# Kernel optimization log

Measured on AMD Instinct MI355X. Metric: run time of the kernel, lower is better.

The kernel has to match this reference:

```python
import jax, jax.numpy as jnp
import numpy as np

NUM_HOP = 3
VOCAB = 32000
D = 512          # embed_dim
MEM = 60         # memory_size (> story_size -> T_A slice branch)
BS = 64
STORY = 50
SENT = 32        # max_sent_size
QLEN = 16


def positional_encoding(J, d):
    # pe[i-1, k-1] = 1 - i/J - (k/d) * (1 - 2*i/J), i in 1..J, k in 1..d
    i = jnp.arange(1, J + 1, dtype=jnp.float32)[:, None]
    k = jnp.arange(1, d + 1, dtype=jnp.float32)[None, :]
    return 1.0 - i / J - (k / d) * (1.0 - 2.0 * i / J)


def setup_inputs() -> dict:
    key = jax.random.key(0)
    kA, kT, kC, kQ = jax.random.split(key, 4)
    # stacked embedding tables A[0..num_hop], each (VOCAB, D), N(0, 0.1)
    A = jax.random.normal(kA, (NUM_HOP + 1, VOCAB, D), dtype=jnp.float32) * 0.1
    T_A = jax.random.normal(kT, (1, MEM, D), dtype=jnp.float32) * 0.1
    context = jax.random.randint(kC, (BS, STORY, SENT), 0, VOCAB)
    query = jax.random.randint(kQ, (BS, QLEN), 0, VOCAB)
    return {"context": context, "query": query, "A": A, "T_A": T_A}


def reference(context, query, A, T_A):
    # padding_idx=0: row 0 of every table is zero
    A = A.at[:, 0, :].set(0.0)
    pe = positional_encoding(SENT, D)              # (SENT, D)

    # query encoding: u = B(query).sum(axis=1), B = A[0]; dropout is identity at eval
    u = A[0][query].sum(axis=1)                    # (BS, D)

    for h in range(NUM_HOP):
        # memory embedding with positional encoding, summed over words
        m = (A[h][context] * pe).sum(axis=2)       # (BS, STORY, D)
        # temporal encoding: memory_size > story_size branch
        m = m + T_A[:, :STORY, :]
        # output embedding (no positional encoding applied in original)
        c = A[h + 1][context].sum(axis=2)          # (BS, STORY, D)
        p = jax.nn.softmax(jnp.einsum('bsd,bd->bs', m, u), axis=1)
        u = u + jnp.einsum('bs,bsd->bd', p, c)

    # W = A[-1].weight.T -> logits = u @ W
    logits = u @ A[NUM_HOP].T                      # (BS, VOCAB)
    return jax.nn.softmax(logits, axis=-1)
```

## Files before the change

kernel.cpp:

```cpp
#include <hip/hip_runtime.h>
#include <math.h>

#define NUM_HOP 3
#define VOCAB   32000
#define DIM     512
#define MEM     60
#define BS      64
#define STORY   50
#define SENT    32
#define QLEN    16

#define SZ      ((size_t)BS * STORY * DIM)
#define TBL     ((size_t)VOCAB * DIM)

typedef short v8s __attribute__((ext_vector_type(8)));
typedef float v4f __attribute__((ext_vector_type(4)));

static __device__ __forceinline__ ushort f2bf(float x) {
    union { float f; unsigned u; } v; v.f = x;
    unsigned r = (v.u + 0x7FFFu + ((v.u >> 16) & 1u)) >> 16;
    return (ushort)r;
}

__global__ __launch_bounds__(128) void k_gather(const float* __restrict__ A,
                                                const int*   __restrict__ ctx,
                                                const int*   __restrict__ query,
                                                float*       __restrict__ mw,
                                                float*       __restrict__ c,
                                                float*       __restrict__ u) {
    const unsigned blk = blockIdx.x;
    const int d = threadIdx.x * 4;
    if (blk >= 4u * BS * STORY) {
        const int b = blk - 4u * BS * STORY;
        const int* q = query + b * QLEN;
        float4 acc = make_float4(0.f, 0.f, 0.f, 0.f);
        for (int t = 0; t < QLEN; ++t) {
            const int idx = q[t];
            if (idx != 0) {
                const float4 a = *(const float4*)(A + (size_t)idx * DIM + d);
                acc.x += a.x; acc.y += a.y; acc.z += a.z; acc.w += a.w;
            }
        }
        *(float4*)(u + (size_t)b * DIM + d) = acc;
        return;
    }
    const unsigned pass = blk / (BS * STORY);
    const unsigned bs   = blk - pass * (BS * STORY);
    const float* table = A + (size_t)pass * TBL;
    const int*   cw    = ctx + bs * SENT;

    float4 m  = make_float4(0.f, 0.f, 0.f, 0.f);
    float4 cc = make_float4(0.f, 0.f, 0.f, 0.f);
    const float invD = 1.0f / (float)DIM;
    #pragma unroll 8
    for (int w = 0; w < SENT; ++w) {
        const int idx = cw[w];
        if (idx == 0) continue;
        const float4 a = *(const float4*)(table + (size_t)idx * DIM + d);
        const float aw = 1.0f - (float)(w + 1) * (1.0f / (float)SENT);
        const float bw = 1.0f - (float)(2 * (w + 1)) * (1.0f / (float)SENT);
        m.x = fmaf(a.x, aw - bw * (float)(d + 1) * invD, m.x);
        m.y = fmaf(a.y, aw - bw * (float)(d + 2) * invD, m.y);
        m.z = fmaf(a.z, aw - bw * (float)(d + 3) * invD, m.z);
        m.w = fmaf(a.w, aw - bw * (float)(d + 4) * invD, m.w);
        cc.x += a.x; cc.y += a.y; cc.z += a.z; cc.w += a.w;
    }
    if (pass < 3) *(float4*)(mw + (size_t)pass * SZ + (size_t)bs * DIM + d) = m;
    if (pass > 0) *(float4*)(c + (size_t)(pass - 1) * SZ + (size_t)bs * DIM + d) = cc;
}

__global__ __launch_bounds__(512) void k_hops(const float* __restrict__ mw,
                                              const float* __restrict__ c,
                                              const float* __restrict__ T_A,
                                              const float* __restrict__ u_g,
                                              ushort*      __restrict__ ubf) {
    const int b    = blockIdx.x;
    const int tid  = threadIdx.x;
    const int wave = tid >> 6;
    const int lane = tid & 63;
    __shared__ float su[DIM];
    __shared__ float sw[64];
    __shared__ float up[8][DIM];

    su[tid] = u_g[(size_t)b * DIM + tid];
    __syncthreads();

    for (int h = 0; h < NUM_HOP; ++h) {
        const float* mwh = mw + (size_t)h * SZ + (size_t)b * STORY * DIM;
        const float* ch  = c  + (size_t)h * SZ + (size_t)b * STORY * DIM;

        const float4 u0 = *(const float4*)(&su[lane * 8]);
        const float4 u1 = *(const float4*)(&su[lane * 8 + 4]);
        for (int s = wave; s < STORY; s += 8) {
            const float* mrow = mwh + (size_t)s * DIM + lane * 8;
            const float* trow = T_A + (size_t)s * DIM + lane * 8;
            const float4 m0 = *(const float4*)(mrow);
            const float4 m1 = *(const float4*)(mrow + 4);
            const float4 t0 = *(const float4*)(trow);
            const float4 t1 = *(const float4*)(trow + 4);
            float p = (m0.x + t0.x) * u0.x + (m0.y + t0.y) * u0.y +
                      (m0.z + t0.z) * u0.z + (m0.w + t0.w) * u0.w +
                      (m1.x + t1.x) * u1.x + (m1.y + t1.y) * u1.y +
                      (m1.z + t1.z) * u1.z + (m1.w + t1.w) * u1.w;
            for (int off = 32; off; off >>= 1) p += __shfl_down(p, off);
            if (lane == 0) sw[s] = p;
        }
        __syncthreads();

        if (tid < 64) {
            const float v = (tid < STORY) ? sw[tid] : -1e30f;
            float mx = v;
            for (int off = 32; off; off >>= 1) mx = fmaxf(mx, __shfl_down(mx, off));
            mx = __shfl(mx, 0);
            const float e = (tid < STORY) ? __expf(v - mx) : 0.f;
            float sm = e;
            for (int off = 32; off; off >>= 1) sm += __shfl_down(sm, off);
            sm = __shfl(sm, 0);
            if (tid < STORY) sw[tid] = e / sm;
        }
        __syncthreads();

        float4 a0 = make_float4(0.f, 0.f, 0.f, 0.f);
        float4 a1 = make_float4(0.f, 0.f, 0.f, 0.f);
        for (int s = wave; s < STORY; s += 8) {
            const float  w    = sw[s];
            const float* crow = ch + (size_t)s * DIM + lane * 8;
            const float4 c0 = *(const float4*)(crow);
            const float4 c1 = *(const float4*)(crow + 4);
            a0.x = fmaf(w, c0.x, a0.x); a0.y = fmaf(w, c0.y, a0.y);
            a0.z = fmaf(w, c0.z, a0.z); a0.w = fmaf(w, c0.w, a0.w);
            a1.x = fmaf(w, c1.x, a1.x); a1.y = fmaf(w, c1.y, a1.y);
            a1.z = fmaf(w, c1.z, a1.z); a1.w = fmaf(w, c1.w, a1.w);
        }
        *(float4*)(&up[wave][lane * 8])     = a0;
        *(float4*)(&up[wave][lane * 8 + 4]) = a1;
        __syncthreads();

        float add = 0.f;
        #pragma unroll
        for (int w = 0; w < 8; ++w) add += up[w][tid];
        su[tid] += add;
        __syncthreads();
    }

    ubf[(size_t)b * DIM + tid] = f2bf(su[tid]);
}

__global__ __launch_bounds__(256) void k_logits(const float*  __restrict__ A3,
                                                const ushort* __restrict__ ubf,
                                                float*        __restrict__ out) {
    __shared__ ushort Abf[64 * 128];
    __shared__ ushort Ubf[64 * 128];
    const int tid  = threadIdx.x;
    const int lane = tid & 63;
    const int wave = tid >> 6;
    const int i16  = lane & 15;
    const int quad = lane >> 4;
    const int row0 = blockIdx.x * 64;

    v4f acc[4];
    #pragma unroll
    for (int nt = 0; nt < 4; ++nt) acc[nt] = (v4f){0.f, 0.f, 0.f, 0.f};

    for (int ko = 0; ko < 4; ++ko) {
        __syncthreads();
        #pragma unroll
        for (int it = 0; it < 4; ++it) {
            const int i = it * 256 + tid;
            const int r = i >> 4, g = i & 15;
            const float* src = A3 + ((size_t)(row0 + r)) * DIM + ko * 128 + g * 8;
            const float4 f0 = *(const float4*)(src);
            const float4 f1 = *(const float4*)(src + 4);
            union { ushort h[8]; uint4 q; } pk;
            pk.h[0] = f2bf(f0.x); pk.h[1] = f2bf(f0.y);
            pk.h[2] = f2bf(f0.z); pk.h[3] = f2bf(f0.w);
            pk.h[4] = f2bf(f1.x); pk.h[5] = f2bf(f1.y);
            pk.h[6] = f2bf(f1.z); pk.h[7] = f2bf(f1.w);
            *(uint4*)(&Abf[r * 128 + ((g ^ (r & 7)) * 8)]) = pk.q;
        }
        #pragma unroll
        for (int it = 0; it < 4; ++it) {
            const int i = it * 256 + tid;
            const int n = i >> 4, g = i & 15;
            const uint4 v = *(const uint4*)(ubf + (size_t)n * DIM + ko * 128 + g * 8);
            *(uint4*)(&Ubf[n * 128 + ((g ^ (n & 7)) * 8)]) = v;
        }
        __syncthreads();

        const int arow = wave * 16 + i16;
        #pragma unroll
        for (int ki = 0; ki < 4; ++ki) {
            const int ga = ki * 4 + quad;
            const v8s a = *(const v8s*)(&Abf[arow * 128 + ((ga ^ (arow & 7)) * 8)]);
            #pragma unroll
            for (int nt = 0; nt < 4; ++nt) {
                const int n = nt * 16 + i16;
                const v8s bb = *(const v8s*)(&Ubf[n * 128 + ((ga ^ (n & 7)) * 8)]);
                acc[nt] = __builtin_amdgcn_mfma_f32_16x16x32_bf16(a, bb, acc[nt], 0, 0, 0);
            }
        }
    }

    const int vbase = row0 + wave * 16 + quad * 4;
    #pragma unroll
    for (int nt = 0; nt < 4; ++nt) {
        const int bcol = nt * 16 + i16;
        #pragma unroll
        for (int r = 0; r < 4; ++r)
            out[(size_t)bcol * VOCAB + vbase + r] = acc[nt][r];
    }
}

__global__ __launch_bounds__(1024) void k_vsm(float* __restrict__ out) {
    const int b   = blockIdx.x;
    const int tid = threadIdx.x;
    float* row = out + (size_t)b * VOCAB;
    __shared__ float red[16];
    __shared__ float bc;

    float x[32];
    #pragma unroll
    for (int k = 0; k < 31; ++k) x[k] = row[tid + k * 1024];
    const bool extra = (tid < VOCAB - 31 * 1024);
    x[31] = extra ? row[tid + 31 * 1024] : -1e30f;

    float mx = -1e30f;
    #pragma unroll
    for (int k = 0; k < 32; ++k) mx = fmaxf(mx, x[k]);
    for (int off = 32; off; off >>= 1) mx = fmaxf(mx, __shfl_down(mx, off));
    if ((tid & 63) == 0) red[tid >> 6] = mx;
    __syncthreads();
    if (tid < 64) {
        float v = (tid < 16) ? red[tid] : -1e30f;
        for (int off = 8; off; off >>= 1) v = fmaxf(v, __shfl_down(v, off));
        if (tid == 0) bc = v;
    }
    __syncthreads();
    mx = bc;
    __syncthreads();

    float sum = 0.f;
    #pragma unroll
    for (int k = 0; k < 32; ++k) { x[k] = __expf(x[k] - mx); sum += x[k]; }
    if (!extra) sum -= x[31];
    for (int off = 32; off; off >>= 1) sum += __shfl_down(sum, off);
    if ((tid & 63) == 0) red[tid >> 6] = sum;
    __syncthreads();
    if (tid < 64) {
        float v = (tid < 16) ? red[tid] : 0.f;
        for (int off = 8; off; off >>= 1) v += __shfl_down(v, off);
        if (tid == 0) bc = v;
    }
    __syncthreads();
    const float inv = 1.0f / bc;

    #pragma unroll
    for (int k = 0; k < 31; ++k) row[tid + k * 1024] = x[k] * inv;
    if (extra) row[tid + 31 * 1024] = x[31] * inv;
}

extern "C" void kernel_launch(void* const* d_in, const int* in_sizes, int n_in,
                              void* d_out, int out_size, void* d_ws, size_t ws_size,
                              hipStream_t stream) {
    const int*   ctx   = (const int*)d_in[0];
    const int*   query = (const int*)d_in[1];
    const float* A     = (const float*)d_in[2];
    const float* T_A   = (const float*)d_in[3];
    float* out = (float*)d_out;

    float*  u   = (float*)d_ws;
    ushort* ubf = (ushort*)(u + (size_t)BS * DIM);
    float*  mw  = (float*)(ubf + (size_t)BS * DIM);
    float*  c   = mw + 3 * SZ;

    k_gather<<<4 * BS * STORY + BS, 128, 0, stream>>>(A, ctx, query, mw, c, u);
    k_hops  <<<BS, 512, 0, stream>>>(mw, c, T_A, u, ubf);
    k_logits<<<VOCAB / 64, 256, 0, stream>>>(A + 3 * TBL, ubf, out);
    k_vsm   <<<BS, 1024, 0, stream>>>(out);
}
```

Before: 455.6 us.

## Fuse all stages into one cooperative persistent kernel with grid syncs

Replaces the four launches with a single cooperative kernel of 512 blocks separated by grid.sync phases: gather, hops overlapped with a bf16 conversion of A[3] into workspace, the MFMA logits GEMM, and a split softmax using per-segment max/sum pairs merged across 8 blocks per row. This is meant to remove launch gaps, move the fp32-to-bf16 conversion off the GEMM critical path onto otherwise idle blocks, and spread the vocab softmax over 512 blocks instead of 64. In exchange it adds grid-wide barriers, an extra bf16 table round trip through memory, and a persistent grid that processes the gather with fewer concurrent blocks.

```diff
diff --git a/kernel.cpp b/kernel.cpp
--- a/kernel.cpp
+++ b/kernel.cpp
@@ -1,5 +1,8 @@
 #include <hip/hip_runtime.h>
+#include <hip/hip_cooperative_groups.h>
 #include <math.h>
+
+namespace cg = cooperative_groups;
 
 #define NUM_HOP 3
 #define VOCAB   32000
@@ -12,6 +15,10 @@
 
 #define SZ      ((size_t)BS * STORY * DIM)
 #define TBL     ((size_t)VOCAB * DIM)
+#define NBLK    512
+#define NTHR    256
+#define NSENT   (4 * BS * STORY)
+#define NTASK   (NSENT + BS)
 
 typedef short v8s __attribute__((ext_vector_type(8)));
 typedef float v4f __attribute__((ext_vector_type(4)));
@@ -22,153 +29,144 @@
     return (ushort)r;
 }
 
-__global__ __launch_bounds__(128) void k_gather(const float* __restrict__ A,
-                                                const int*   __restrict__ ctx,
-                                                const int*   __restrict__ query,
-                                                float*       __restrict__ mw,
-                                                float*       __restrict__ c,
-                                                float*       __restrict__ u) {
-    const unsigned blk = blockIdx.x;
-    const int d = threadIdx.x * 4;
-    if (blk >= 4u * BS * STORY) {
-        const int b = blk - 4u * BS * STORY;
-        const int* q = query + b * QLEN;
-        float4 acc = make_float4(0.f, 0.f, 0.f, 0.f);
-        for (int t = 0; t < QLEN; ++t) {
-            const int idx = q[t];
-            if (idx != 0) {
-                const float4 a = *(const float4*)(A + (size_t)idx * DIM + d);
-                acc.x += a.x; acc.y += a.y; acc.z += a.z; acc.w += a.w;
-            }
-        }
-        *(float4*)(u + (size_t)b * DIM + d) = acc;
-        return;
+union __align__(16) SMem {
+    struct { float su[DIM]; float sw[64]; float up[4][DIM]; } hop;
+    struct { ushort a[64 * 128]; ushort u[64 * 128]; } log;
+    struct { float red[8]; } r;
+};
+
+__global__ __launch_bounds__(NTHR, 2)
+void k_fused(const float* __restrict__ A,
+             const int*   __restrict__ ctx,
+             const int*   __restrict__ query,
+             const float* __restrict__ T_A,
+             float*       __restrict__ mw,
+             float*       __restrict__ c,
+             float*       __restrict__ u,
+             ushort*      __restrict__ ubf,
+             ushort*      __restrict__ a3bf,
+             float*       __restrict__ pairs,
+             float*       __restrict__ out) {
+    cg::grid_group grid = cg::this_grid();
+    __shared__ SMem sm;
+    const int tid = threadIdx.x;
+    const int blk = blockIdx.x;
+
+    {
+        const int hb = blk * 2 + (tid >> 7);
+        const int lt = tid & 127;
+        const int d  = lt * 4;
+        const float invD = 1.0f / (float)DIM;
+        for (int t = hb; t < NTASK; t += 2 * NBLK) {
+            if (t < NSENT) {
+                const int pass = t / (BS * STORY);
+                const int bs   = t - pass * (BS * STORY);
+                const float* table = A + (size_t)pass * TBL;
+                const int*   cw    = ctx + bs * SENT;
+                float4 m  = make_float4(0.f, 0.f, 0.f, 0.f);
+                float4 cc = make_float4(0.f, 0.f, 0.f, 0.f);
+                #pragma unroll 8
+                for (int w = 0; w < SENT; ++w) {
+                    const int idx = cw[w];
+                    if (idx == 0) continue;
+                    const float4 a = *(const float4*)(table + (size_t)idx * DIM + d);
+                    const float aw = 1.0f - (float)(w + 1) * (1.0f / (float)SENT);
+                    const float bw = 1.0f - (float)(2 * (w + 1)) * (1.0f / (float)SENT);
+                    m.x = fmaf(a.x, aw - bw * (float)(d + 1) * invD, m.x);
+                    m.y = fmaf(a.y, aw - bw * (float)(d + 2) * invD, m.y);
+                    m.z = fmaf(a.z, aw - bw * (float)(d + 3) * invD, m.z);
+                    m.w = fmaf(a.w, aw - bw * (float)(d + 4) * invD, m.w);
+                    cc.x += a.x; cc.y += a.y; cc.z += a.z; cc.w += a.w;
+                }
+                if (pass < 3)
+                    *(float4*)(mw + (size_t)pass * SZ + (size_t)bs * DIM + d) = m;
+                if (pass > 0)
+                    *(float4*)(c + (size_t)(pass - 1) * SZ + (size_t)bs * DIM + d) = cc;
+            } else {
+                const int b = t - NSENT;
+                const int* q = query + b * QLEN;
+                float4 acc = make_float4(0.f, 0.f, 0.f, 0.f);
+                for (int tt = 0; tt < QLEN; ++tt) {
+                    const int idx = q[tt];
+                    if (idx != 0) {
+                        const float4 a = *(const float4*)(A + (size_t)idx * DIM + d);
+                        acc.x += a.x; acc.y += a.y; acc.z += a.z; acc.w += a.w;
+                    }
+                }
+                *(float4*)(u + (size_t)b * DIM + d) = acc;
+            }
+        }
     }
-    const unsigned pass = blk / (BS * STORY);
-    const unsigned bs   = blk - pass * (BS * STORY);
-    const float* table = A + (size_t)pass * TBL;
-    const int*   cw    = ctx + bs * SENT;
-
-    float4 m  = make_float4(0.f, 0.f, 0.f, 0.f);
-    float4 cc = make_float4(0.f, 0.f, 0.f, 0.f);
-    const float invD = 1.0f / (float)DIM;
-    #pragma unroll 8
-    for (int w = 0; w < SENT; ++w) {
-        const int idx = cw[w];
-        if (idx == 0) continue;
-        const float4 a = *(const float4*)(table + (size_t)idx * DIM + d);
-        const float aw = 1.0f - (float)(w + 1) * (1.0f / (float)SENT);
-        const float bw = 1.0f - (float)(2 * (w + 1)) * (1.0f / (float)SENT);
-        m.x = fmaf(a.x, aw - bw * (float)(d + 1) * invD, m.x);
-        m.y = fmaf(a.y, aw - bw * (float)(d + 2) * invD, m.y);
-        m.z = fmaf(a.z, aw - bw * (float)(d + 3) * invD, m.z);
-        m.w = fmaf(a.w, aw - bw * (float)(d + 4) * invD, m.w);
-        cc.x += a.x; cc.y += a.y; cc.z += a.z; cc.w += a.w;
-    }
-    if (pass < 3) *(float4*)(mw + (size_t)pass * SZ + (size_t)bs * DIM + d) = m;
-    if (pass > 0) *(float4*)(c + (size_t)(pass - 1) * SZ + (size_t)bs * DIM + d) = cc;
-}
-
-__global__ __launch_bounds__(512) void k_hops(const float* __restrict__ mw,
-                                              const float* __restrict__ c,
-                                              const float* __restrict__ T_A,
-                                              const float* __restrict__ u_g,
-                                              ushort*      __restrict__ ubf) {
-    const int b    = blockIdx.x;
-    const int tid  = threadIdx.x;
-    const int wave = tid >> 6;
-    const int lane = tid & 63;
-    __shared__ float su[DIM];
-    __shared__ float sw[64];
-    __shared__ float up[8][DIM];
-
-    su[tid] = u_g[(size_t)b * DIM + tid];
-    __syncthreads();
-
-    for (int h = 0; h < NUM_HOP; ++h) {
-        const float* mwh = mw + (size_t)h * SZ + (size_t)b * STORY * DIM;
-        const float* ch  = c  + (size_t)h * SZ + (size_t)b * STORY * DIM;
-
-        const float4 u0 = *(const float4*)(&su[lane * 8]);
-        const float4 u1 = *(const float4*)(&su[lane * 8 + 4]);
-        for (int s = wave; s < STORY; s += 8) {
-            const float* mrow = mwh + (size_t)s * DIM + lane * 8;
-            const float* trow = T_A + (size_t)s * DIM + lane * 8;
-            const float4 m0 = *(const float4*)(mrow);
-            const float4 m1 = *(const float4*)(mrow + 4);
-            const float4 t0 = *(const float4*)(trow);
-            const float4 t1 = *(const float4*)(trow + 4);
-            float p = (m0.x + t0.x) * u0.x + (m0.y + t0.y) * u0.y +
-                      (m0.z + t0.z) * u0.z + (m0.w + t0.w) * u0.w +
-                      (m1.x + t1.x) * u1.x + (m1.y + t1.y) * u1.y +
-                      (m1.z + t1.z) * u1.z + (m1.w + t1.w) * u1.w;
-            for (int off = 32; off; off >>= 1) p += __shfl_down(p, off);
-            if (lane == 0) sw[s] = p;
-        }
+    grid.sync();
+
+    if (blk < BS) {
+        const int b    = blk;
+        const int wave = tid >> 6;
+        const int lane = tid & 63;
+        sm.hop.su[tid]       = u[(size_t)b * DIM + tid];
+        sm.hop.su[tid + 256] = u[(size_t)b * DIM + tid + 256];
         __syncthreads();
-
-        if (tid < 64) {
-            const float v = (tid < STORY) ? sw[tid] : -1e30f;
-            float mx = v;
-            for (int off = 32; off; off >>= 1) mx = fmaxf(mx, __shfl_down(mx, off));
-            mx = __shfl(mx, 0);
-            const float e = (tid < STORY) ? __expf(v - mx) : 0.f;
-            float sm = e;
-            for (int off = 32; off; off >>= 1) sm += __shfl_down(sm, off);
-            sm = __shfl(sm, 0);
-            if (tid < STORY) sw[tid] = e / sm;
-        }
-        __syncthreads();
-
-        float4 a0 = make_float4(0.f, 0.f, 0.f, 0.f);
-        float4 a1 = make_float4(0.f, 0.f, 0.f, 0.f);
-        for (int s = wave; s < STORY; s += 8) {
-            const float  w    = sw[s];
-            const float* crow = ch + (size_t)s * DIM + lane * 8;
-            const float4 c0 = *(const float4*)(crow);
-            const float4 c1 = *(const float4*)(crow + 4);
-            a0.x = fmaf(w, c0.x, a0.x); a0.y = fmaf(w, c0.y, a0.y);
-            a0.z = fmaf(w, c0.z, a0.z); a0.w = fmaf(w, c0.w, a0.w);
-            a1.x = fmaf(w, c1.x, a1.x); a1.y = fmaf(w, c1.y, a1.y);
-            a1.z = fmaf(w, c1.z, a1.z); a1.w = fmaf(w, c1.w, a1.w);
-        }
-        *(float4*)(&up[wave][lane * 8])     = a0;
-        *(float4*)(&up[wave][lane * 8 + 4]) = a1;
-        __syncthreads();
-
-        float add = 0.f;
-        #pragma unroll
-        for (int w = 0; w < 8; ++w) add += up[w][tid];
-        su[tid] += add;
-        __syncthreads();
-    }
-
-    ubf[(size_t)b * DIM + tid] = f2bf(su[tid]);
-}
-
-__global__ __launch_bounds__(256) void k_logits(const float*  __restrict__ A3,
-                                                const ushort* __restrict__ ubf,
-                                                float*        __restrict__ out) {
-    __shared__ ushort Abf[64 * 128];
-    __shared__ ushort Ubf[64 * 128];
-    const int tid  = threadIdx.x;
-    const int lane = tid & 63;
-    const int wave = tid >> 6;
-    const int i16  = lane & 15;
-    const int quad = lane >> 4;
-    const int row0 = blockIdx.x * 64;
-
-    v4f acc[4];
-    #pragma unroll
-    for (int nt = 0; nt < 4; ++nt) acc[nt] = (v4f){0.f, 0.f, 0.f, 0.f};
-
-    for (int ko = 0; ko < 4; ++ko) {
-        __syncthreads();
-        #pragma unroll
-        for (int it = 0; it < 4; ++it) {
-            const int i = it * 256 + tid;
-            const int r = i >> 4, g = i & 15;
-            const float* src = A3 + ((size_t)(row0 + r)) * DIM + ko * 128 + g * 8;
+        for (int h = 0; h < NUM_HOP; ++h) {
+            const float* mwh = mw + (size_t)h * SZ + (size_t)b * STORY * DIM;
+            const float* ch  = c  + (size_t)h * SZ + (size_t)b * STORY * DIM;
+            const float4 u0 = *(const float4*)(&sm.hop.su[lane * 8]);
+            const float4 u1 = *(const float4*)(&sm.hop.su[lane * 8 + 4]);
+            for (int s = wave; s < STORY; s += 4) {
+                const float* mrow = mwh + (size_t)s * DIM + lane * 8;
+                const float* trow = T_A + (size_t)s * DIM + lane * 8;
+                const float4 m0 = *(const float4*)(mrow);
+                const float4 m1 = *(const float4*)(mrow + 4);
+                const float4 t0 = *(const float4*)(trow);
+                const float4 t1 = *(const float4*)(trow + 4);
+                float p = (m0.x + t0.x) * u0.x + (m0.y + t0.y) * u0.y +
+                          (m0.z + t0.z) * u0.z + (m0.w + t0.w) * u0.w +
+                          (m1.x + t1.x) * u1.x + (m1.y + t1.y) * u1.y +
+                          (m1.z + t1.z) * u1.z + (m1.w + t1.w) * u1.w;
+                for (int off = 32; off; off >>= 1) p += __shfl_down(p, off);
+                if (lane == 0) sm.hop.sw[s] = p;
+            }
+            __syncthreads();
+            if (tid < 64) {
+                const float v = (tid < STORY) ? sm.hop.sw[tid] : -1e30f;
+                float mx = v;
+                for (int off = 32; off; off >>= 1) mx = fmaxf(mx, __shfl_down(mx, off));
+                mx = __shfl(mx, 0);
+                const float e = (tid < STORY) ? __expf(v - mx) : 0.f;
+                float smm = e;
+                for (int off = 32; off; off >>= 1) smm += __shfl_down(smm, off);
+                smm = __shfl(smm, 0);
+                if (tid < STORY) sm.hop.sw[tid] = e / smm;
+            }
+            __syncthreads();
+            float4 a0 = make_float4(0.f, 0.f, 0.f, 0.f);
+            float4 a1 = make_float4(0.f, 0.f, 0.f, 0.f);
+            for (int s = wave; s < STORY; s += 4) {
+                const float  w    = sm.hop.sw[s];
+                const float* crow = ch + (size_t)s * DIM + lane * 8;
+                const float4 c0 = *(const float4*)(crow);
+                const float4 c1 = *(const float4*)(crow + 4);
+                a0.x = fmaf(w, c0.x, a0.x); a0.y = fmaf(w, c0.y, a0.y);
+                a0.z = fmaf(w, c0.z, a0.z); a0.w = fmaf(w, c0.w, a0.w);
+                a1.x = fmaf(w, c1.x, a1.x); a1.y = fmaf(w, c1.y, a1.y);
+                a1.z = fmaf(w, c1.z, a1.z); a1.w = fmaf(w, c1.w, a1.w);
+            }
+            *(float4*)(&sm.hop.up[wave][lane * 8])     = a0;
+            *(float4*)(&sm.hop.up[wave][lane * 8 + 4]) = a1;
+            __syncthreads();
+            sm.hop.su[tid] += sm.hop.up[0][tid] + sm.hop.up[1][tid] +
+                              sm.hop.up[2][tid] + sm.hop.up[3][tid];
+            sm.hop.su[tid + 256] += sm.hop.up[0][tid + 256] + sm.hop.up[1][tid + 256] +
+                                    sm.hop.up[2][tid + 256] + sm.hop.up[3][tid + 256];
+            __syncthreads();
+        }
+        ubf[(size_t)b * DIM + tid]       = f2bf(sm.hop.su[tid]);
+        ubf[(size_t)b * DIM + tid + 256] = f2bf(sm.hop.su[tid + 256]);
+    } else {
+        const float* A3 = A + 3 * TBL;
+        const size_t n8 = TBL / 8;
+        for (size_t i = (size_t)(blk - BS) * NTHR + tid; i < n8;
+             i += (size_t)(NBLK - BS) * NTHR) {
+            const float* src = A3 + i * 8;
             const float4 f0 = *(const float4*)(src);
             const float4 f1 = *(const float4*)(src + 4);
             union { ushort h[8]; uint4 q; } pk;
@@ -176,87 +174,99 @@
             pk.h[2] = f2bf(f0.z); pk.h[3] = f2bf(f0.w);
             pk.h[4] = f2bf(f1.x); pk.h[5] = f2bf(f1.y);
             pk.h[6] = f2bf(f1.z); pk.h[7] = f2bf(f1.w);
-            *(uint4*)(&Abf[r * 128 + ((g ^ (r & 7)) * 8)]) = pk.q;
-        }
+            *(uint4*)(a3bf + i * 8) = pk.q;
+        }
+    }
+    grid.sync();
+
+    if (blk < VOCAB / 64) {
+        const int lane = tid & 63;
+        const int wave = tid >> 6;
+        const int i16  = lane & 15;
+        const int quad = lane >> 4;
+        const int row0 = blk * 64;
+        v4f acc[4];
         #pragma unroll
-        for (int it = 0; it < 4; ++it) {
-            const int i = it * 256 + tid;
-            const int n = i >> 4, g = i & 15;
-            const uint4 v = *(const uint4*)(ubf + (size_t)n * DIM + ko * 128 + g * 8);
-            *(uint4*)(&Ubf[n * 128 + ((g ^ (n & 7)) * 8)]) = v;
-        }
-        __syncthreads();
-
-        const int arow = wave * 16 + i16;
+        for (int nt = 0; nt < 4; ++nt) acc[nt] = (v4f){0.f, 0.f, 0.f, 0.f};
+        for (int ko = 0; ko < 4; ++ko) {
+            __syncthreads();
+            #pragma unroll
+            for (int it = 0; it < 4; ++it) {
+                const int i = it * 256 + tid;
+                const int r = i >> 4, g = i & 15;
+                const uint4 v = *(const uint4*)(a3bf + (size_t)(row0 + r) * DIM + ko * 128 + g * 8);
+                *(uint4*)(&sm.log.a[r * 128 + ((g ^ (r & 7)) * 8)]) = v;
+            }
+            #pragma unroll
+            for (int it = 0; it < 4; ++it) {
+                const int i = it * 256 + tid;
+                const int n = i >> 4, g = i & 15;
+                const uint4 v = *(const uint4*)(ubf + (size_t)n * DIM + ko * 128 + g * 8);
+                *(uint4*)(&sm.log.u[n * 128 + ((g ^ (n & 7)) * 8)]) = v;
+            }
+            __syncthreads();
+            const int arow = wave * 16 + i16;
+            #pragma unroll
+            for (int ki = 0; ki < 4; ++ki) {
+                const int ga = ki * 4 + quad;
+                const v8s a = *(const v8s*)(&sm.log.a[arow * 128 + ((ga ^ (arow & 7)) * 8)]);
+                #pragma unroll
+                for (int nt = 0; nt < 4; ++nt) {
+                    const int n = nt * 16 + i16;
+                    const v8s bb = *(const v8s*)(&sm.log.u[n * 128 + ((ga ^ (n & 7)) * 8)]);
+                    acc[nt] = __builtin_amdgcn_mfma_f32_16x16x32_bf16(a, bb, acc[nt], 0, 0, 0);
+                }
+            }
+        }
+        const int vbase = row0 + wave * 16 + quad * 4;
         #pragma unroll
-        for (int ki = 0; ki < 4; ++ki) {
-            const int ga = ki * 4 + quad;
-            const v8s a = *(const v8s*)(&Abf[arow * 128 + ((ga ^ (arow & 7)) * 8)]);
-            #pragma unroll
-            for (int nt = 0; nt < 4; ++nt) {
-                const int n = nt * 16 + i16;
-                const v8s bb = *(const v8s*)(&Ubf[n * 128 + ((ga ^ (n & 7)) * 8)]);
-                acc[nt] = __builtin_amdgcn_mfma_f32_16x16x32_bf16(a, bb, acc[nt], 0, 0, 0);
-            }
+        for (int nt = 0; nt < 4; ++nt) {
+            const int bcol = nt * 16 + i16;
+            #pragma unroll
+            for (int r = 0; r < 4; ++r)
+                out[(size_t)bcol * VOCAB + vbase + r] = acc[nt][r];
         }
     }
-
-    const int vbase = row0 + wave * 16 + quad * 4;
-    #pragma unroll
-    for (int nt = 0; nt < 4; ++nt) {
-        const int bcol = nt * 16 + i16;
-        #pragma unroll
-        for (int r = 0; r < 4; ++r)
-            out[(size_t)bcol * VOCAB + vbase + r] = acc[nt][r];
-    }
-}
-
-__global__ __launch_bounds__(1024) void k_vsm(float* __restrict__ out) {
-    const int b   = blockIdx.x;
-    const int tid = threadIdx.x;
-    float* row = out + (size_t)b * VOCAB;
-    __shared__ float red[16];
-    __shared__ float bc;
-
-    float x[32];
-    #pragma unroll
-    for (int k = 0; k < 31; ++k) x[k] = row[tid + k * 1024];
-    const bool extra = (tid < VOCAB - 31 * 1024);
-    x[31] = extra ? row[tid + 31 * 1024] : -1e30f;
+    grid.sync();
+
+    const int vb  = blk >> 3;
+    const int seg = blk & 7;
+    float* row = out + (size_t)vb * VOCAB + seg * 4000;
+    float x[16];
+    #pragma unroll
+    for (int k = 0; k < 15; ++k) x[k] = row[tid + k * 256];
+    const bool extra = (tid < 4000 - 15 * 256);
+    x[15] = extra ? row[tid + 15 * 256] : -1e30f;
 
     float mx = -1e30f;
     #pragma unroll
-    for (int k = 0; k < 32; ++k) mx = fmaxf(mx, x[k]);
+    for (int k = 0; k < 16; ++k) mx = fmaxf(mx, x[k]);
     for (int off = 32; off; off >>= 1) mx = fmaxf(mx, __shfl_down(mx, off));
-    if ((tid & 63) == 0) red[tid >> 6] = mx;
+    if ((tid & 63) == 0) sm.r.red[tid >> 6] = mx;
     __syncthreads();
-    if (tid < 64) {
-        float v = (tid < 16) ? red[tid] : -1e30f;
-        for (int off = 8; off; off >>= 1) v = fmaxf(v, __shfl_down(v, off));
-        if (tid == 0) bc = v;
-    }
+    mx = fmaxf(fmaxf(sm.r.red[0], sm.r.red[1]), fmaxf(sm.r.red[2], sm.r.red[3]));
     __syncthreads();
-    mx = bc;
+    float sum = 0.f;
+    #pragma unroll
+    for (int k = 0; k < 16; ++k) { x[k] = __expf(x[k] - mx); sum += x[k]; }
+    for (int off = 32; off; off >>= 1) sum += __shfl_down(sum, off);
+    if ((tid & 63) == 0) sm.r.red[4 + (tid >> 6)] = sum;
     __syncthreads();
-
-    float sum = 0.f;
-    #pragma unroll
-    for (int k = 0; k < 32; ++k) { x[k] = __expf(x[k] - mx); sum += x[k]; }
-    if (!extra) sum -= x[31];
-    for (int off = 32; off; off >>= 1) sum += __shfl_down(sum, off);
-    if ((tid & 63) == 0) red[tid >> 6] = sum;
-    __syncthreads();
-    if (tid < 64) {
-        float v = (tid < 16) ? red[tid] : 0.f;
-        for (int off = 8; off; off >>= 1) v += __shfl_down(v, off);
-        if (tid == 0) bc = v;
-    }
-    __syncthreads();
-    const float inv = 1.0f / bc;
-
-    #pragma unroll
-    for (int k = 0; k < 31; ++k) row[tid + k * 1024] = x[k] * inv;
-    if (extra) row[tid + 31 * 1024] = x[31] * inv;
+    sum = sm.r.red[4] + sm.r.red[5] + sm.r.red[6] + sm.r.red[7];
+    if (tid == 0) { pairs[blk * 2] = mx; pairs[blk * 2 + 1] = sum; }
+    grid.sync();
+
+    float M = -1e30f;
+    #pragma unroll
+    for (int j = 0; j < 8; ++j) M = fmaxf(M, pairs[(vb * 8 + j) * 2]);
+    float S = 0.f;
+    #pragma unroll
+    for (int j = 0; j < 8; ++j)
+        S += pairs[(vb * 8 + j) * 2 + 1] * __expf(pairs[(vb * 8 + j) * 2] - M);
+    const float scale = __expf(mx - M) / S;
+    #pragma unroll
+    for (int k = 0; k < 15; ++k) row[tid + k * 256] = x[k] * scale;
+    if (extra) row[tid + 15 * 256] = x[15] * scale;
 }
 
 extern "C" void kernel_launch(void* const* d_in, const int* in_sizes, int n_in,
@@ -268,13 +278,16 @@
     const float* T_A   = (const float*)d_in[3];
     float* out = (float*)d_out;
 
-    float*  u   = (float*)d_ws;
-    ushort* ubf = (ushort*)(u + (size_t)BS * DIM);
-    float*  mw  = (float*)(ubf + (size_t)BS * DIM);
-    float*  c   = mw + 3 * SZ;
-
-    k_gather<<<4 * BS * STORY + BS, 128, 0, stream>>>(A, ctx, query, mw, c, u);
-    k_hops  <<<BS, 512, 0, stream>>>(mw, c, T_A, u, ubf);
-    k_logits<<<VOCAB / 64, 256, 0, stream>>>(A + 3 * TBL, ubf, out);
-    k_vsm   <<<BS, 1024, 0, stream>>>(out);
+    float*  u     = (float*)d_ws;
+    float*  pairs = u + (size_t)BS * DIM;
+    ushort* ubf   = (ushort*)(pairs + 1024);
+    ushort* a3bf  = ubf + (size_t)BS * DIM;
+    float*  mw    = (float*)(a3bf + TBL);
+    float*  c     = mw + 3 * SZ;
+
+    void* args[] = {(void*)&A, (void*)&ctx, (void*)&query, (void*)&T_A,
+                    (void*)&mw, (void*)&c, (void*)&u, (void*)&ubf,
+                    (void*)&a3bf, (void*)&pairs, (void*)&out};
+    hipLaunchCooperativeKernel((void*)k_fused, dim3(NBLK), dim3(NTHR),
+                               args, 0, stream);
 }
```

Measured after the change: 897.1 us. 96.9% more time.
